# Kernel optimization log

Measured on AMD Instinct MI355X. Metric: run time of the kernel, lower is better.

The kernel has to match this reference:

```python
import jax, jax.numpy as jnp
import numpy as np

ALPHA, BETA = 0.7, 0.3
EPS = 1e-12  # F.normalize eps

def _l2norm(x):
    n = jnp.linalg.norm(x, axis=-1, keepdims=True)
    return x / jnp.maximum(n, EPS)

def setup_inputs() -> dict:
    key = jax.random.key(0)
    k = jax.random.split(key, 6)
    B, L, D, A = 8, 2048, 128, 1024
    return {
        "new_emb1": jax.random.normal(k[0], (B, L, D), jnp.float32),
        "new_emb2": jax.random.normal(k[1], (B, L, D), jnp.float32),
        "global_emb1": jax.random.normal(k[2], (B, D), jnp.float32),
        "global_emb2": jax.random.normal(k[3], (B, D), jnp.float32),
        "lddt_scores": jax.random.uniform(k[4], (B, L), jnp.float32),
        "alignment_mask": jnp.ones((B, L), jnp.float32),
        "alignment": jax.random.randint(k[5], (B, A, 2), 0, L, jnp.int64 if jax.config.jax_enable_x64 else jnp.int32),
    }

def reference(new_emb1, new_emb2, global_emb1, global_emb2, lddt_scores, alignment_mask, alignment):
    B = new_emb1.shape[0]
    # --- per-residue LDDT loss ---
    e1 = _l2norm(new_emb1)  # [B,L,D]
    e2 = _l2norm(new_emb2)
    b_idx = jnp.arange(B)[:, None]            # [B,1]
    i_idx = alignment[..., 0]                 # [B,A]
    j_idx = alignment[..., 1]
    v1 = e1[b_idx, i_idx]                     # [B,A,D] gather of aligned rows
    v2 = e2[b_idx, j_idx]                     # [B,A,D]
    sim = jnp.einsum('bad,bad->ba', v1, v2)   # == similarity[b,i,j] of bmm
    lddt_aligned = lddt_scores[b_idx, i_idx]  # [B,A]
    residue_loss = jnp.mean((sim - lddt_aligned) ** 2)  # per-batch MSE then batch mean (equal A per batch)
    # --- global contrastive-style loss ---
    g1 = _l2norm(global_emb1)
    g2 = _l2norm(global_emb2)
    cos = jnp.sum(g1 * g2, axis=-1)           # cosine of unit vectors == dot
    global_loss = jnp.mean((cos - 0.8) ** 2)
    total_loss = ALPHA * residue_loss + BETA * global_loss
    return (total_loss, residue_loss, global_loss)
```

## Files before the change

### kernel.cpp

```cpp
#include <hip/hip_runtime.h>
#include <math.h>


constexpr int B_ = 8;
constexpr int L_ = 2048;
constexpr int D_ = 128;
constexpr int A_ = 1024;
constexpr int NPAIR = B_ * A_;
constexpr float ALPHA = 0.7f;
constexpr float BETA  = 0.3f;
constexpr float EPS   = 1e-12f;

__device__ __forceinline__ float wave_reduce_sum(float v) {
    #pragma unroll
    for (int m = 32; m >= 1; m >>= 1) v += __shfl_xor(v, m, 64);
    return v;
}

__global__ void residue_kernel(const float* __restrict__ e1,
                               const float* __restrict__ e2,
                               const float* __restrict__ lddt,
                               const int*   __restrict__ align,
                               float*       __restrict__ ws) {
    const int wave = (blockIdx.x * blockDim.x + threadIdx.x) >> 6;
    const int lane = threadIdx.x & 63;
    if (wave >= NPAIR) return;
    const int b = wave >> 10;
    const int i = align[wave * 2 + 0];
    const int j = align[wave * 2 + 1];

    const float2* r1 = reinterpret_cast<const float2*>(e1 + (size_t)(b * L_ + i) * D_);
    const float2* r2 = reinterpret_cast<const float2*>(e2 + (size_t)(b * L_ + j) * D_);
    const float2 a1 = r1[lane];
    const float2 a2 = r2[lane];

    float dot = a1.x * a2.x + a1.y * a2.y;
    float n1  = a1.x * a1.x + a1.y * a1.y;
    float n2  = a2.x * a2.x + a2.y * a2.y;
    dot = wave_reduce_sum(dot);
    n1  = wave_reduce_sum(n1);
    n2  = wave_reduce_sum(n2);

    if (lane == 0) {
        const float sim = dot / (fmaxf(sqrtf(n1), EPS) * fmaxf(sqrtf(n2), EPS));
        const float d   = sim - lddt[b * L_ + i];
        ws[wave] = d * d;
    }
}

__global__ void global_kernel(const float* __restrict__ g1,
                              const float* __restrict__ g2,
                              float*       __restrict__ ws) {
    const int wave = threadIdx.x >> 6;
    const int lane = threadIdx.x & 63;

    const float2* r1 = reinterpret_cast<const float2*>(g1 + (size_t)wave * D_);
    const float2* r2 = reinterpret_cast<const float2*>(g2 + (size_t)wave * D_);
    const float2 a1 = r1[lane];
    const float2 a2 = r2[lane];

    float dot = a1.x * a2.x + a1.y * a2.y;
    float n1  = a1.x * a1.x + a1.y * a1.y;
    float n2  = a2.x * a2.x + a2.y * a2.y;
    dot = wave_reduce_sum(dot);
    n1  = wave_reduce_sum(n1);
    n2  = wave_reduce_sum(n2);

    if (lane == 0) {
        const float cosv = dot / (fmaxf(sqrtf(n1), EPS) * fmaxf(sqrtf(n2), EPS));
        const float d    = cosv - 0.8f;
        ws[NPAIR + wave] = d * d;
    }
}

__global__ void finalize_kernel(const float* __restrict__ ws,
                                float*       __restrict__ out) {
    __shared__ float s_res[4];
    __shared__ float s_glob[4];
    const int tid  = threadIdx.x;
    const int wave = tid >> 6;
    const int lane = tid & 63;

    float r = 0.0f;
    for (int idx = tid; idx < NPAIR; idx += 256) r += ws[idx];
    float g = (tid < B_) ? ws[NPAIR + tid] : 0.0f;

    r = wave_reduce_sum(r);
    g = wave_reduce_sum(g);
    if (lane == 0) { s_res[wave] = r; s_glob[wave] = g; }
    __syncthreads();

    if (tid == 0) {
        const float res  = s_res[0] + s_res[1] + s_res[2] + s_res[3];
        const float glob = s_glob[0] + s_glob[1] + s_glob[2] + s_glob[3];
        const float residue_loss = res  / (float)NPAIR;
        const float global_loss  = glob / (float)B_;
        out[0] = ALPHA * residue_loss + BETA * global_loss;
        out[1] = residue_loss;
        out[2] = global_loss;
    }
}

extern "C" void kernel_launch(void* const* d_in, const int* in_sizes, int n_in,
                              void* d_out, int out_size, void* d_ws, size_t ws_size,
                              hipStream_t stream) {
    const float* e1    = (const float*)d_in[0];
    const float* e2    = (const float*)d_in[1];
    const float* g1    = (const float*)d_in[2];
    const float* g2    = (const float*)d_in[3];
    const float* lddt  = (const float*)d_in[4];
    const int*   align = (const int*)d_in[6];
    float* ws  = (float*)d_ws;
    float* out = (float*)d_out;

    residue_kernel<<<NPAIR / 4, 256, 0, stream>>>(e1, e2, lddt, align, ws);
    global_kernel<<<1, 512, 0, stream>>>(g1, g2, ws);
    finalize_kernel<<<1, 256, 0, stream>>>(ws, out);
}
```

Baseline: 83.49 us.

## Fuse residue, global and finalize kernels into one with atomic last-block reduction

Merges the three kernels into a single launch. Each wave now handles four aligned pairs with their gathers issued up front, and block 0 also computes the global loss. The final reduction uses float atomics plus a completion counter, where the last block writes the outputs. This removes two kernel launches and the workspace round trip. In exchange it adds a memset launch, makes the sum order nondeterministic, and relies on the counter being reset to zero by that memset.

```diff
diff --git a/kernel.cpp b/kernel.cpp
--- a/kernel.cpp
+++ b/kernel.cpp
@@ -7,6 +7,7 @@
 constexpr int D_ = 128;
 constexpr int A_ = 1024;
 constexpr int NPAIR = B_ * A_;
+constexpr int BLOCKS = 512;
 constexpr float ALPHA = 0.7f;
 constexpr float BETA  = 0.3f;
 constexpr float EPS   = 1e-12f;
@@ -17,87 +18,88 @@
     return v;
 }
 
-__global__ void residue_kernel(const float* __restrict__ e1,
-                               const float* __restrict__ e2,
-                               const float* __restrict__ lddt,
-                               const int*   __restrict__ align,
-                               float*       __restrict__ ws) {
-    const int wave = (blockIdx.x * blockDim.x + threadIdx.x) >> 6;
-    const int lane = threadIdx.x & 63;
-    if (wave >= NPAIR) return;
-    const int b = wave >> 10;
-    const int i = align[wave * 2 + 0];
-    const int j = align[wave * 2 + 1];
-
-    const float2* r1 = reinterpret_cast<const float2*>(e1 + (size_t)(b * L_ + i) * D_);
-    const float2* r2 = reinterpret_cast<const float2*>(e2 + (size_t)(b * L_ + j) * D_);
-    const float2 a1 = r1[lane];
-    const float2 a2 = r2[lane];
-
-    float dot = a1.x * a2.x + a1.y * a2.y;
-    float n1  = a1.x * a1.x + a1.y * a1.y;
-    float n2  = a2.x * a2.x + a2.y * a2.y;
-    dot = wave_reduce_sum(dot);
-    n1  = wave_reduce_sum(n1);
-    n2  = wave_reduce_sum(n2);
-
-    if (lane == 0) {
-        const float sim = dot / (fmaxf(sqrtf(n1), EPS) * fmaxf(sqrtf(n2), EPS));
-        const float d   = sim - lddt[b * L_ + i];
-        ws[wave] = d * d;
-    }
-}
-
-__global__ void global_kernel(const float* __restrict__ g1,
-                              const float* __restrict__ g2,
-                              float*       __restrict__ ws) {
-    const int wave = threadIdx.x >> 6;
-    const int lane = threadIdx.x & 63;
-
-    const float2* r1 = reinterpret_cast<const float2*>(g1 + (size_t)wave * D_);
-    const float2* r2 = reinterpret_cast<const float2*>(g2 + (size_t)wave * D_);
-    const float2 a1 = r1[lane];
-    const float2 a2 = r2[lane];
-
-    float dot = a1.x * a2.x + a1.y * a2.y;
-    float n1  = a1.x * a1.x + a1.y * a1.y;
-    float n2  = a2.x * a2.x + a2.y * a2.y;
-    dot = wave_reduce_sum(dot);
-    n1  = wave_reduce_sum(n1);
-    n2  = wave_reduce_sum(n2);
-
-    if (lane == 0) {
-        const float cosv = dot / (fmaxf(sqrtf(n1), EPS) * fmaxf(sqrtf(n2), EPS));
-        const float d    = cosv - 0.8f;
-        ws[NPAIR + wave] = d * d;
-    }
-}
-
-__global__ void finalize_kernel(const float* __restrict__ ws,
-                                float*       __restrict__ out) {
-    __shared__ float s_res[4];
+__global__ __launch_bounds__(256) void fused_kernel(
+        const float* __restrict__ e1, const float* __restrict__ e2,
+        const float* __restrict__ g1, const float* __restrict__ g2,
+        const float* __restrict__ lddt, const int* __restrict__ align,
+        float* __restrict__ ws, float* __restrict__ out) {
+    __shared__ float s_part[4];
     __shared__ float s_glob[4];
     const int tid  = threadIdx.x;
-    const int wave = tid >> 6;
+    const int w    = tid >> 6;
     const int lane = tid & 63;
 
-    float r = 0.0f;
-    for (int idx = tid; idx < NPAIR; idx += 256) r += ws[idx];
-    float g = (tid < B_) ? ws[NPAIR + tid] : 0.0f;
+    const int pair0 = (blockIdx.x * 4 + w) * 4;
+    const int b     = pair0 >> 10;
+    const int4 ij01 = *reinterpret_cast<const int4*>(align + (size_t)pair0 * 2);
+    const int4 ij23 = *reinterpret_cast<const int4*>(align + (size_t)pair0 * 2 + 4);
+    const int iidx[4] = { ij01.x, ij01.z, ij23.x, ij23.z };
+    const int jidx[4] = { ij01.y, ij01.w, ij23.y, ij23.w };
 
-    r = wave_reduce_sum(r);
-    g = wave_reduce_sum(g);
-    if (lane == 0) { s_res[wave] = r; s_glob[wave] = g; }
+    const float* e1b = e1 + (size_t)b * L_ * D_;
+    const float* e2b = e2 + (size_t)b * L_ * D_;
+    const float* lb  = lddt + b * L_;
+
+    float2 a1[4], a2[4];
+    #pragma unroll
+    for (int p = 0; p < 4; ++p) {
+        a1[p] = reinterpret_cast<const float2*>(e1b + (size_t)iidx[p] * D_)[lane];
+        a2[p] = reinterpret_cast<const float2*>(e2b + (size_t)jidx[p] * D_)[lane];
+    }
+
+    float local = 0.0f;
+    #pragma unroll
+    for (int p = 0; p < 4; ++p) {
+        float dot = a1[p].x * a2[p].x + a1[p].y * a2[p].y;
+        float n1  = a1[p].x * a1[p].x + a1[p].y * a1[p].y;
+        float n2  = a2[p].x * a2[p].x + a2[p].y * a2[p].y;
+        dot = wave_reduce_sum(dot);
+        n1  = wave_reduce_sum(n1);
+        n2  = wave_reduce_sum(n2);
+        const float sim = dot / (fmaxf(sqrtf(n1), EPS) * fmaxf(sqrtf(n2), EPS));
+        const float d   = sim - lb[iidx[p]];
+        local += d * d;
+    }
+    if (lane == 0) s_part[w] = local;
+
+    if (blockIdx.x == 0) {
+        float gsum = 0.0f;
+        #pragma unroll
+        for (int r = 0; r < 2; ++r) {
+            const int bb = w + 4 * r;
+            const float2 x = reinterpret_cast<const float2*>(g1 + (size_t)bb * D_)[lane];
+            const float2 y = reinterpret_cast<const float2*>(g2 + (size_t)bb * D_)[lane];
+            float dot = x.x * y.x + x.y * y.y;
+            float n1  = x.x * x.x + x.y * x.y;
+            float n2  = y.x * y.x + y.y * y.y;
+            dot = wave_reduce_sum(dot);
+            n1  = wave_reduce_sum(n1);
+            n2  = wave_reduce_sum(n2);
+            const float c = dot / (fmaxf(sqrtf(n1), EPS) * fmaxf(sqrtf(n2), EPS)) - 0.8f;
+            gsum += c * c;
+        }
+        if (lane == 0) s_glob[w] = gsum;
+    }
     __syncthreads();
 
     if (tid == 0) {
-        const float res  = s_res[0] + s_res[1] + s_res[2] + s_res[3];
-        const float glob = s_glob[0] + s_glob[1] + s_glob[2] + s_glob[3];
-        const float residue_loss = res  / (float)NPAIR;
-        const float global_loss  = glob / (float)B_;
-        out[0] = ALPHA * residue_loss + BETA * global_loss;
-        out[1] = residue_loss;
-        out[2] = global_loss;
+        float* acc = ws;
+        unsigned* cnt = reinterpret_cast<unsigned*>(ws) + 2;
+        atomicAdd(&acc[0], s_part[0] + s_part[1] + s_part[2] + s_part[3]);
+        if (blockIdx.x == 0)
+            atomicAdd(&acc[1], s_glob[0] + s_glob[1] + s_glob[2] + s_glob[3]);
+        __threadfence();
+        const unsigned old = atomicAdd(cnt, 1u);
+        if (old == (unsigned)gridDim.x - 1u) {
+            __threadfence();
+            const float res  = atomicAdd(&acc[0], 0.0f);
+            const float glob = atomicAdd(&acc[1], 0.0f);
+            const float residue_loss = res  / (float)NPAIR;
+            const float global_loss  = glob / (float)B_;
+            out[0] = ALPHA * residue_loss + BETA * global_loss;
+            out[1] = residue_loss;
+            out[2] = global_loss;
+        }
     }
 }
 
@@ -113,7 +115,6 @@
     float* ws  = (float*)d_ws;
     float* out = (float*)d_out;
 
-    residue_kernel<<<NPAIR / 4, 256, 0, stream>>>(e1, e2, lddt, align, ws);
-    global_kernel<<<1, 512, 0, stream>>>(g1, g2, ws);
-    finalize_kernel<<<1, 256, 0, stream>>>(ws, out);
+    hipMemsetAsync(ws, 0, 16, stream);
+    fused_kernel<<<BLOCKS, 256, 0, stream>>>(e1, e2, g1, g2, lddt, align, ws, out);
 }
```

After: 86.89 us. 4.1% more time.
